# Performance work log

Measured on AMD Instinct MI355X. Metric: run time of the kernel, lower is better.

The kernel has to match this reference:

```python
import jax, jax.numpy as jnp
import numpy as np

V_THRESH = 0.3

@jax.custom_vjp
def spike(x):
    return (x > 0).astype(x.dtype)

def _spike_fwd(x):
    return spike(x), x

def _spike_bwd(x, g):
    # rectangular straight-through surrogate gradient (pass grad where |x| < 0.5)
    return (g * (jnp.abs(x) < 0.5).astype(g.dtype),)

spike.defvjp(_spike_fwd, _spike_bwd)


def setup_inputs() -> dict:
    key = jax.random.key(0)
    B, T, H = 128, 2048, 128
    k1, = jax.random.split(key, 1)
    x_seq = jax.random.normal(k1, (B, T, H), dtype=jnp.float32)
    v0 = jnp.zeros((B, H), dtype=jnp.float32)
    z0 = jnp.zeros((B, H), dtype=jnp.float32)
    decay_raw = jnp.zeros((H,), dtype=jnp.float32)  # nn.initializers.constant(0.0)
    return {"x_seq": x_seq, "v0": v0, "z0": z0, "decay_raw": decay_raw}


def reference(x_seq, v0, z0, decay_raw):
    # LIF recurrence: v_t = v_{t-1} * decay * (1 - z_{t-1}) + x_t ; z_t = spike(v_t - v_thresh)
    decay = jax.nn.sigmoid(decay_raw)  # (H,)

    def step(carry, x_t):
        v, z = carry
        v = v * decay * (1.0 - z) + x_t
        z_out = spike(v - V_THRESH)
        return (v, z_out), z_out

    x_tb = jnp.swapaxes(x_seq, 0, 1)  # [T, B, H] for lax.scan over time
    (_, _), spk_tb = jax.lax.scan(step, (v0, z0), x_tb)
    return jnp.swapaxes(spk_tb, 0, 1)  # [B, T, H]
```

## Files before the change

kernel.cpp:

```cpp
#include <hip/hip_runtime.h>
#include <math.h>


constexpr int Bdim = 128;
constexpr int Tdim = 2048;
constexpr int Hdim = 128;
constexpr int HW   = 64;
constexpr int Ut   = 64;
constexpr int NT   = Tdim / Ut;
constexpr int NX   = 5;
constexpr int NZ   = 3;
constexpr float VTH = 0.3f;


typedef const __attribute__((address_space(1))) void* gptr_t;
typedef __attribute__((address_space(3))) void* lptr_t;

__device__ __forceinline__ void cfence() { asm volatile("" ::: "memory"); }

__global__ __launch_bounds__(256) void lif_kernel(
    const float* __restrict__ x,
    const float* __restrict__ v0,
    const float* __restrict__ z0,
    const float* __restrict__ decay_raw,
    float* __restrict__ out)
{
    __shared__ float xbuf[NX][Ut][HW];
    __shared__ float zbuf[NZ][Ut][HW];
    __shared__ int   flags[8];

    volatile int* vf = (volatile int*)flags;

    const int tid  = threadIdx.x;
    const int wave = tid >> 6;
    const int lane = tid & 63;
    const int blk  = blockIdx.x;
    const int b    = blk >> 1;
    const int h0   = (blk & 1) * HW;

    if (tid < 8) flags[tid] = 0;
    __syncthreads();

    const float* xbase = x   + (size_t)b * Tdim * Hdim + h0;
    float*       obase = out + (size_t)b * Tdim * Hdim + h0;
    const int sub = (lane >> 4) * Hdim + (lane & 15) * 4;

    if (wave == 1 || wave == 3) {
        const int par = (wave == 1) ? 0 : 1;
        for (int i = 0; i < NT / 2; ++i) {
            const int k = 2 * i + par;
            while (vf[2] < k - NX + 1) __builtin_amdgcn_s_sleep(2);
            cfence();
            const float* g = xbase + (size_t)k * Ut * Hdim + sub;
            float* lbase = &xbuf[k % NX][0][0];
            #pragma unroll
            for (int j = 0; j < Ut / 4; ++j) {
                __builtin_amdgcn_global_load_lds(
                    (gptr_t)(const void*)(g + (size_t)(4 * j) * Hdim),
                    (lptr_t)(void*)(lbase + 4 * j * HW),
                    16, 0, 0);
            }
            asm volatile("s_waitcnt vmcnt(16)" ::: "memory");
            if (lane == 0) vf[par] = i;
        }
        asm volatile("s_waitcnt vmcnt(0)" ::: "memory");
        if (lane == 0) vf[par] = NT / 2;
    } else if (wave == 0) {
        const float decay = 1.0f / (1.0f + expf(-decay_raw[h0 + lane]));
        float v = v0[b * Hdim + h0 + lane];
        float z = z0[b * Hdim + h0 + lane];

        for (int k = 0; k < NT; ++k) {
            const int need = (k >> 1) + 1;
            while (vf[k & 1] < need) __builtin_amdgcn_s_sleep(2);
            while (vf[4] < k - NZ + 1) __builtin_amdgcn_s_sleep(2);
            cfence();
            const int xb = k % NX, zb = k % NZ;
            #pragma unroll 16
            for (int t = 0; t < Ut; ++t) {
                const float xv = xbuf[xb][t][lane];
                const float a  = v * decay + 0.0f;
                const float s  = a + xv;
                v = (z > 0.5f) ? xv : s;
                z = (v > VTH) ? 1.0f : 0.0f;
                zbuf[zb][t][lane] = z;
            }
            asm volatile("s_waitcnt lgkmcnt(0)" ::: "memory");
            if (lane == 0) { vf[3] = k + 1; vf[2] = k + 1; }
        }
    } else {
        for (int k = 0; k < NT; ++k) {
            while (vf[3] < k + 1) __builtin_amdgcn_s_sleep(2);
            cfence();
            const int zb = k % NZ;
            float* op = obase + (size_t)k * Ut * Hdim;
            #pragma unroll
            for (int s = 0; s < Ut / 4; ++s) {
                const int row = 4 * s + (lane >> 4);
                const int col = (lane & 15) * 4;
                const float4 vv = *(const float4*)&zbuf[zb][row][col];
                *(float4*)(op + (size_t)row * Hdim + col) = vv;
            }
            cfence();
            if (lane == 0) vf[4] = k + 1;
            asm volatile("s_waitcnt vmcnt(16)" ::: "memory");
        }
    }
}

extern "C" void kernel_launch(void* const* d_in, const int* in_sizes, int n_in,
                              void* d_out, int out_size, void* d_ws, size_t ws_size,
                              hipStream_t stream) {
    const float* x         = (const float*)d_in[0];
    const float* v0        = (const float*)d_in[1];
    const float* z0        = (const float*)d_in[2];
    const float* decay_raw = (const float*)d_in[3];
    float* out = (float*)d_out;

    lif_kernel<<<Bdim * Hdim / HW, 256, 0, stream>>>(x, v0, z0, decay_raw, out);
}
```

Baseline: 246.6 us.

## Use six register-staged loader waves with per-chunk ready flags

Replaces the two loader waves that used direct global-to-LDS loads with six loader waves. Each of these loads a 64-step chunk into registers, writes it to LDS and sets a per-chunk ready flag, with the x ring buffer grown to six slots. The store wave now reads the whole z chunk into registers and releases the buffer before issuing its global stores. The intent is more memory-level parallelism feeding the serial recurrence wave, and an earlier release of zbuf. The cost is 512 threads per block, more LDS and more register pressure, which may reduce occupancy.

```diff
diff --git a/kernel.cpp b/kernel.cpp
--- a/kernel.cpp
+++ b/kernel.cpp
@@ -8,17 +8,16 @@
 constexpr int HW   = 64;
 constexpr int Ut   = 64;
 constexpr int NT   = Tdim / Ut;
-constexpr int NX   = 5;
+constexpr int NX   = 6;
 constexpr int NZ   = 3;
+constexpr int NLOAD = 6;
 constexpr float VTH = 0.3f;
 
+__device__ __forceinline__ void lgkm_fence() {
+    asm volatile("s_waitcnt lgkmcnt(0)" ::: "memory");
+}
 
-typedef const __attribute__((address_space(1))) void* gptr_t;
-typedef __attribute__((address_space(3))) void* lptr_t;
-
-__device__ __forceinline__ void cfence() { asm volatile("" ::: "memory"); }
-
-__global__ __launch_bounds__(256) void lif_kernel(
+__global__ __launch_bounds__(512) void lif_kernel(
     const float* __restrict__ x,
     const float* __restrict__ v0,
     const float* __restrict__ z0,
@@ -27,7 +26,7 @@
 {
     __shared__ float xbuf[NX][Ut][HW];
     __shared__ float zbuf[NZ][Ut][HW];
-    __shared__ int   flags[8];
+    __shared__ int   flags[NT + 8];
 
     volatile int* vf = (volatile int*)flags;
 
@@ -38,72 +37,64 @@
     const int b    = blk >> 1;
     const int h0   = (blk & 1) * HW;
 
-    if (tid < 8) flags[tid] = 0;
+    for (int i = tid; i < NT + 8; i += 512) flags[i] = 0;
     __syncthreads();
 
     const float* xbase = x   + (size_t)b * Tdim * Hdim + h0;
     float*       obase = out + (size_t)b * Tdim * Hdim + h0;
-    const int sub = (lane >> 4) * Hdim + (lane & 15) * 4;
+    const int r_sub = lane >> 4;
+    const int c_sub = (lane & 15) * 4;
+    const int sub   = r_sub * Hdim + c_sub;
 
-    if (wave == 1 || wave == 3) {
-        const int par = (wave == 1) ? 0 : 1;
-        for (int i = 0; i < NT / 2; ++i) {
-            const int k = 2 * i + par;
-            while (vf[2] < k - NX + 1) __builtin_amdgcn_s_sleep(2);
-            cfence();
+    if (wave >= 1 && wave <= NLOAD) {
+        for (int k = wave - 1; k < NT; k += NLOAD) {
+            while (vf[NT] < k - NX + 1) __builtin_amdgcn_s_sleep(2);
             const float* g = xbase + (size_t)k * Ut * Hdim + sub;
-            float* lbase = &xbuf[k % NX][0][0];
+            float4 tmp[16];
             #pragma unroll
-            for (int j = 0; j < Ut / 4; ++j) {
-                __builtin_amdgcn_global_load_lds(
-                    (gptr_t)(const void*)(g + (size_t)(4 * j) * Hdim),
-                    (lptr_t)(void*)(lbase + 4 * j * HW),
-                    16, 0, 0);
-            }
-            asm volatile("s_waitcnt vmcnt(16)" ::: "memory");
-            if (lane == 0) vf[par] = i;
+            for (int j = 0; j < 16; ++j)
+                tmp[j] = *(const float4*)(g + (size_t)(4 * j) * Hdim);
+            const int xb = k % NX;
+            #pragma unroll
+            for (int j = 0; j < 16; ++j)
+                *(float4*)&xbuf[xb][4 * j + r_sub][c_sub] = tmp[j];
+            lgkm_fence();
+            if (lane == 0) vf[k] = 1;
         }
-        asm volatile("s_waitcnt vmcnt(0)" ::: "memory");
-        if (lane == 0) vf[par] = NT / 2;
     } else if (wave == 0) {
         const float decay = 1.0f / (1.0f + expf(-decay_raw[h0 + lane]));
         float v = v0[b * Hdim + h0 + lane];
         float z = z0[b * Hdim + h0 + lane];
 
         for (int k = 0; k < NT; ++k) {
-            const int need = (k >> 1) + 1;
-            while (vf[k & 1] < need) __builtin_amdgcn_s_sleep(2);
-            while (vf[4] < k - NZ + 1) __builtin_amdgcn_s_sleep(2);
-            cfence();
+            while (vf[k] == 0)           __builtin_amdgcn_s_sleep(1);
+            while (vf[NT + 2] < k - NZ + 1) __builtin_amdgcn_s_sleep(1);
             const int xb = k % NX, zb = k % NZ;
             #pragma unroll 16
             for (int t = 0; t < Ut; ++t) {
                 const float xv = xbuf[xb][t][lane];
-                const float a  = v * decay + 0.0f;
-                const float s  = a + xv;
+                const float s  = v * decay + xv;
                 v = (z > 0.5f) ? xv : s;
                 z = (v > VTH) ? 1.0f : 0.0f;
                 zbuf[zb][t][lane] = z;
             }
-            asm volatile("s_waitcnt lgkmcnt(0)" ::: "memory");
-            if (lane == 0) { vf[3] = k + 1; vf[2] = k + 1; }
+            lgkm_fence();
+            if (lane == 0) { vf[NT + 1] = k + 1; vf[NT] = k + 1; }
         }
     } else {
         for (int k = 0; k < NT; ++k) {
-            while (vf[3] < k + 1) __builtin_amdgcn_s_sleep(2);
-            cfence();
+            while (vf[NT + 1] < k + 1) __builtin_amdgcn_s_sleep(1);
             const int zb = k % NZ;
-            float* op = obase + (size_t)k * Ut * Hdim;
+            float4 vv[16];
             #pragma unroll
-            for (int s = 0; s < Ut / 4; ++s) {
-                const int row = 4 * s + (lane >> 4);
-                const int col = (lane & 15) * 4;
-                const float4 vv = *(const float4*)&zbuf[zb][row][col];
-                *(float4*)(op + (size_t)row * Hdim + col) = vv;
-            }
-            cfence();
-            if (lane == 0) vf[4] = k + 1;
-            asm volatile("s_waitcnt vmcnt(16)" ::: "memory");
+            for (int s = 0; s < 16; ++s)
+                vv[s] = *(const float4*)&zbuf[zb][4 * s + r_sub][c_sub];
+            lgkm_fence();
+            if (lane == 0) vf[NT + 2] = k + 1;
+            float* op = obase + (size_t)k * Ut * Hdim + sub;
+            #pragma unroll
+            for (int s = 0; s < 16; ++s)
+                *(float4*)(op + (size_t)(4 * s) * Hdim) = vv[s];
         }
     }
 }
@@ -117,5 +108,5 @@
     const float* decay_raw = (const float*)d_in[3];
     float* out = (float*)d_out;
 
-    lif_kernel<<<Bdim * Hdim / HW, 256, 0, stream>>>(x, v0, z0, decay_raw, out);
+    lif_kernel<<<Bdim * Hdim / HW, 512, 0, stream>>>(x, v0, z0, decay_raw, out);
 }
```

After: 254.7 us. 3.3% more time.
